# Optimization experiments

Measured on AMD Instinct MI355X. Metric: run time of the kernel, lower is better.

The kernel has to match this reference:

```python
import jax, jax.numpy as jnp
import numpy as np

B, T, N = 1024, 5, 6        # batch, seq_len (fixed by conv3d1 kernel), max_node_num
D, E, M, L = 192, 12, 12, 512  # node feat, edge feat, message size, link hidden
P = 2                        # propagate_layers
O = 6                        # big_attr_classes / conv3d out channels


def setup_inputs() -> dict:
    key = jax.random.key(0)
    ks = jax.random.split(key, 16)
    w = lambda k, shp: jax.random.normal(k, shp, jnp.float32) * 0.02
    return {
        "node_resnet": jax.random.normal(ks[0], (B, T, D, N), jnp.float32),
        "pos": jax.random.normal(ks[1], (B, T, N, 6), jnp.float32),
        "attmat": jax.random.randint(ks[2], (B, T, N, N), 0, 2).astype(jnp.int32),
        "link_w1": w(ks[3], (L, E)), "link_b1": jnp.zeros((L,), jnp.float32),
        "link_w2": w(ks[4], (1, L)), "link_b2": jnp.zeros((1,), jnp.float32),
        "msg_Wh": w(ks[5], (M, D)), "msg_We": w(ks[6], (M, E)), "msg_b": jnp.zeros((M,), jnp.float32),
        "gru_Wih": w(ks[7], (3 * D, M)), "gru_Whh": w(ks[8], (3 * D, D)),
        "gru_bih": jnp.zeros((3 * D,), jnp.float32), "gru_bhh": jnp.zeros((3 * D,), jnp.float32),
        "conv1_w": w(ks[9], (O, D, T, N, 1)), "conv1_b": jnp.zeros((O,), jnp.float32),
        "conv2_w": w(ks[10], (O, O)), "conv2_b": jnp.zeros((O,), jnp.float32),
    }


def reference(node_resnet, pos, attmat, link_w1, link_b1, link_w2, link_b2,
              msg_Wh, msg_We, msg_b, gru_Wih, gru_Whh, gru_bih, gru_bhh,
              conv1_w, conv1_b, conv2_w, conv2_b):
    # edge features: e[b,t,:,i,j] = cat(pos_i, pos_j) where ATTMAT==1 and i!=j
    eye = jnp.eye(N, dtype=bool)
    mask = (attmat == 1) & (~eye)[None, None]                      # [B,T,N,N]
    pi = jnp.broadcast_to(pos[:, :, :, None, :], (B, T, N, N, 6))
    pj = jnp.broadcast_to(pos[:, :, None, :, :], (B, T, N, N, 6))
    e = jnp.concatenate([pi, pj], -1) * mask[..., None]            # [B,T,N,N,E]
    e = jnp.moveaxis(e, -1, 2)                                     # [B,T,E,N,N]

    def link(es):  # GraphConv link function: 1x1 conv stack -> scalar edge logit
        hmid = jax.nn.relu(jnp.einsum('btcij,oc->btoij', es, link_w1)
                           + link_b1[None, None, :, None, None])
        return jnp.einsum('btoij,po->btpij', hmid, link_w2)[:, :, 0] + link_b2[0]  # [B,T,N,N]

    h = node_resnet                                                # [B,T,D,N]
    edge_state = e
    for _ in range(P):
        adj = jax.nn.sigmoid(link(edge_state))                     # [B,T,N,N] gate (i=target, j=source)
        # message: relu(Wh h_j + We e_ij + b), gated by sigmoid adjacency
        mh = jnp.einsum('btcj,oc->btoj', h, msg_Wh)                # [B,T,M,N]
        me = jnp.einsum('btcij,oc->btoij', e, msg_We)              # [B,T,M,N,N]
        m = jax.nn.relu(mh[:, :, :, None, :] + me + msg_b[None, None, :, None, None])
        m = adj[:, :, None, :, :] * m                              # gated messages
        edge_state = m                                             # next-round edge hidden state
        msum = m.sum(-1)                                           # aggregate over source j: [B,T,M,N]
        # GRU update per node (PyTorch gate order r, z, n)
        x = jnp.moveaxis(msum, 2, -1)                              # [B,T,N,M]
        hh = jnp.moveaxis(h, 2, -1)                                # [B,T,N,D]
        gi = x @ gru_Wih.T + gru_bih
        gh = hh @ gru_Whh.T + gru_bhh
        ir, iz, inn = jnp.split(gi, 3, -1)
        hr, hz, hn = jnp.split(gh, 3, -1)
        r = jax.nn.sigmoid(ir + hr)
        z = jax.nn.sigmoid(iz + hz)
        n = jnp.tanh(inn + r * hn)
        hh = (1.0 - z) * n + z * hh
        h = jnp.moveaxis(hh, -1, 2)                                # [B,T,D,N]

    # conv3d1 kernel (5,6,1) spans full (T,N) -> single contraction per batch
    out = jax.nn.relu(jnp.einsum('btdn,odtn->bo', h, conv1_w[..., 0]) + conv1_b)
    out = out @ conv2_w.T + conv2_b                                # conv3d2 is 1x1x1
    return out.reshape(B, O, 1, 1, 1)
```

## Files before the change

### kernel.cpp

```cpp
#include <hip/hip_runtime.h>
#include <math.h>

#define NB 1024
#define TT 5
#define NN 6
#define DD 192
#define EE 12
#define MM 12
#define LL 512
#define OO 6
#define GOUT 768
#define KPAD 224
#define NKT (KPAD/32)
#define NJT (GOUT/16)

#define ROWS 30
#define HP 196
#define LNKPU 20
#define GRUPU 116

typedef __attribute__((ext_vector_type(8))) _Float16 f16x8;
typedef __attribute__((ext_vector_type(2))) _Float16 h2;
typedef __attribute__((ext_vector_type(4))) float f32x4;

__device__ __forceinline__ float dot4(float4 a, float4 b) {
  return a.x*b.x + a.y*b.y + a.z*b.z + a.w*b.w;
}
__device__ __forceinline__ unsigned short f2h(float f) {
  _Float16 h = (_Float16)f;
  unsigned short s; __builtin_memcpy(&s, &h, 2); return s;
}
__device__ __forceinline__ unsigned int pkrtz(float a, float b) {
  auto v = __builtin_amdgcn_cvt_pkrtz(a, b);
  return __builtin_bit_cast(unsigned int, v);
}
__device__ __forceinline__ float fsig(float x) {
  float e = __expf(-x);
  return __builtin_amdgcn_rcpf(1.f + e);
}
__device__ __forceinline__ float ftanh(float x) {
  float e = __expf(-2.f * x);
  return 2.f * __builtin_amdgcn_rcpf(1.f + e) - 1.f;
}

__global__ void k_pack(const float* __restrict__ Wih, const float* __restrict__ Whh,
                       const float* __restrict__ bih, const float* __restrict__ bhh,
                       unsigned short* __restrict__ Bh, float* __restrict__ bias768)
{
  int idx = blockIdx.x * 256 + threadIdx.x;
  if (idx < GOUT) {
    int c = idx; float b;
    if (c < 384)      b = bih[c] + bhh[c];
    else if (c < 576) b = bih[c];
    else              b = bhh[c - 192];
    bias768[c] = b;
  }
  if (idx >= NJT*NKT*512) return;
  int e = idx & 7, l = (idx >> 3) & 63;
  int rem = idx >> 9, kt = rem % NKT, j = rem / NKT;
  int k = kt*32 + ((l >> 4) << 3) + e;
  int c = j*16 + (l & 15);
  float v = 0.f;
  if (k < 204) {
    if (c < 384)      v = (k < 12) ? Wih[c*MM + k] : Whh[(size_t)c*DD + (k-12)];
    else if (c < 576) v = (k < 12) ? Wih[c*MM + k] : 0.f;
    else              v = (k < 12) ? 0.f : Whh[(size_t)(c-192)*DD + (k-12)];
  }
  Bh[idx] = f2h(v);
}

__global__ void k_pack_link(const float* __restrict__ w1, const float* __restrict__ b1,
                            unsigned short* __restrict__ BLh)
{
  int idx = blockIdx.x * 256 + threadIdx.x;
  if (idx >= 32*512) return;
  int e = idx & 7, l = (idx >> 3) & 63, nt = idx >> 9;
  int k = ((l >> 4) << 3) + e;
  int c = nt*16 + (l & 15);
  float v = 0.f;
  if (k < 12)       v = w1[c*EE + k];
  else if (k == 12) v = b1[c];
  BLh[idx] = f2h(v);
}

__global__ __launch_bounds__(256, 2)
void k_fused(const float* __restrict__ nr, const float* __restrict__ pos,
             const int* __restrict__ attmat,
             const unsigned short* __restrict__ BLh,
             const float* __restrict__ lw2, const float* __restrict__ lb2,
             const float* __restrict__ msg_Wh, const float* __restrict__ msg_We,
             const float* __restrict__ msg_b,
             const unsigned short* __restrict__ Bh, const float* __restrict__ bias768,
             const float* __restrict__ conv1_w, const float* __restrict__ conv1_b,
             const float* __restrict__ conv2_w, const float* __restrict__ conv2_b,
             float* __restrict__ out)
{
  __shared__ __align__(16) float sh_h[ROWS][HP];
  __shared__ __align__(16) unsigned int sh_e[180][6];
  __shared__ __align__(16) unsigned int sh_m[180][6];
  __shared__ __align__(16) float sh_mh[ROWS][MM];
  __shared__ float sh_adj[192];
  __shared__ float sh_w2[LL];
  __shared__ __align__(16) unsigned int sh_we[MM][6];
  __shared__ __align__(16) unsigned int shA[192*LNKPU];
  __shared__ float red[4][OO];

  const int tid = threadIdx.x;
  const int b = blockIdx.x;
  const int lane = tid & 63, wid = tid >> 6;
  const int col = lane & 15, quad = lane >> 4;

  for (int i = tid; i < TT*DD*NN; i += 256) {
    int t = i / (DD*NN), rem = i % (DD*NN);
    int d = rem / NN, n = rem % NN;
    sh_h[t*NN + n][d] = nr[(size_t)b*TT*DD*NN + i];
  }
  for (int idx = tid; idx < 180*6; idx += 256) {
    int e = idx / 6, p = idx % 6;
    int t = e / 36, ij = e % 36;
    int i_ = ij / NN, j_ = ij % NN;
    bool msk = (attmat[(b*TT + t)*36 + ij] == 1) && (i_ != j_);
    int srcn = (p < 3) ? i_ : j_;
    int c0   = (p < 3) ? 2*p : 2*p - 6;
    const float* pb = pos + (((size_t)(b*TT + t))*NN + srcn)*6;
    float a0 = msk ? pb[c0] : 0.f, a1 = msk ? pb[c0+1] : 0.f;
    sh_e[e][p] = pkrtz(a0, a1);
  }
  for (int idx = tid; idx < MM*6; idx += 256) {
    int o = idx / 6, p = idx % 6;
    sh_we[o][p] = pkrtz(msg_We[o*EE + 2*p], msg_We[o*EE + 2*p + 1]);
  }
  for (int i = tid; i < LL; i += 256) sh_w2[i] = lw2[i];
  __syncthreads();

  for (int L = 0; L < 2; ++L) {
    for (int idx = tid; idx < 192*16; idx += 256) {
      int r = idx >> 4, p = idx & 15;
      unsigned int v = 0;
      if (r < 180) {
        if (p < 6)       v = (L == 0) ? sh_e[r][p] : sh_m[r][p];
        else if (p == 6) v = 0x00003C00u;
      }
      shA[r*LNKPU + p] = v;
    }
    __syncthreads();

    {
      f16x8 am[3];
      #pragma unroll
      for (int mtl = 0; mtl < 3; ++mtl)
        am[mtl] = *(const f16x8*)((const char*)shA
                    + ((wid*3 + mtl)*16 + col)*(LNKPU*4) + quad*16);
      float s[3][4];
      #pragma unroll
      for (int mtl = 0; mtl < 3; ++mtl)
        #pragma unroll
        for (int q = 0; q < 4; ++q) s[mtl][q] = 0.f;
      for (int nt = 0; nt < 32; ++nt) {
        f16x8 bh = *(const f16x8*)(BLh + nt*512 + lane*8);
        float w2v = sh_w2[nt*16 + col];
        #pragma unroll
        for (int mtl = 0; mtl < 3; ++mtl) {
          f32x4 acc = (f32x4)0.f;
          acc = __builtin_amdgcn_mfma_f32_16x16x32_f16(am[mtl], bh, acc, 0, 0, 0);
          #pragma unroll
          for (int q = 0; q < 4; ++q)
            s[mtl][q] += w2v * fmaxf(acc[q], 0.f);
        }
      }
      #pragma unroll
      for (int mtl = 0; mtl < 3; ++mtl)
        #pragma unroll
        for (int q = 0; q < 4; ++q) {
          float v = s[mtl][q];
          v += __shfl_xor(v, 1); v += __shfl_xor(v, 2);
          v += __shfl_xor(v, 4); v += __shfl_xor(v, 8);
          s[mtl][q] = v;
        }
      if (col == 0) {
        float b2 = lb2[0];
        #pragma unroll
        for (int mtl = 0; mtl < 3; ++mtl)
          #pragma unroll
          for (int q = 0; q < 4; ++q)
            sh_adj[wid*48 + mtl*16 + quad*4 + q] = fsig(s[mtl][q] + b2);
      }
    }
    __syncthreads();

    for (int idx = tid; idx < ROWS*MM; idx += 256) {
      int r = idx / MM, o = idx % MM;
      const float4* wrow = (const float4*)(msg_Wh + (size_t)o*DD);
      const float4* hrow = (const float4*)&sh_h[r][0];
      float acc = msg_b[o];
      #pragma unroll 8
      for (int d4 = 0; d4 < DD/4; ++d4) acc += dot4(wrow[d4], hrow[d4]);
      sh_mh[r][o] = acc;
    }
    __syncthreads();

    for (int idx = tid; idx < 180*6; idx += 256) {
      int e = idx / 6, op = idx % 6;
      int t = e / 36, j_ = e % 6;
      h2 a2 = {(_Float16)0.f, (_Float16)0.f};
      h2 b2 = {(_Float16)0.f, (_Float16)0.f};
      #pragma unroll
      for (int p = 0; p < 6; ++p) {
        h2 ev = __builtin_bit_cast(h2, sh_e[e][p]);
        a2 += __builtin_bit_cast(h2, sh_we[2*op][p]) * ev;
        b2 += __builtin_bit_cast(h2, sh_we[2*op+1][p]) * ev;
      }
      float me0 = (float)a2[0] + (float)a2[1];
      float me1 = (float)b2[0] + (float)b2[1];
      float mh0 = sh_mh[t*NN + j_][2*op];
      float mh1 = sh_mh[t*NN + j_][2*op+1];
      float adj = sh_adj[e];
      sh_m[e][op] = pkrtz(adj * fmaxf(mh0 + me0, 0.f),
                          adj * fmaxf(mh1 + me1, 0.f));
    }
    __syncthreads();

    for (int idx = tid; idx < 32*(KPAD/2); idx += 256) {
      int r = idx / (KPAD/2), kp = idx % (KPAD/2);
      unsigned int v = 0;
      if (r < ROWS) {
        if (kp < 6) {
          int t = r / NN, i_ = r % NN;
          const unsigned int* mrow = &sh_m[t*36 + i_*NN][kp];
          float a0 = 0.f, a1 = 0.f;
          #pragma unroll
          for (int j = 0; j < 6; ++j) {
            h2 mv = __builtin_bit_cast(h2, mrow[j*6]);
            a0 += (float)mv[0]; a1 += (float)mv[1];
          }
          v = pkrtz(a0, a1);
        } else if (kp < 102) {
          float2 hv = *(const float2*)&sh_h[r][2*kp - 12];
          v = pkrtz(hv.x, hv.y);
        }
      }
      shA[r*GRUPU + kp] = v;
    }
    __syncthreads();

    {
      const char* ahb = (const char*)shA + col*(GRUPU*4) + quad*16;
      #pragma unroll 1
      for (int i = 0; i < 3; ++i) {
        const int jR = wid*3 + i;
        const int jZ = 12 + wid*3 + i;
        const int jI = 24 + wid*3 + i;
        const int jH = 36 + wid*3 + i;
        f32x4 aR0 = (f32x4)0.f, aR1 = (f32x4)0.f;
        f32x4 aZ0 = (f32x4)0.f, aZ1 = (f32x4)0.f;
        f32x4 aI0 = (f32x4)0.f, aI1 = (f32x4)0.f;
        f32x4 aH0 = (f32x4)0.f, aH1 = (f32x4)0.f;
        #pragma unroll
        for (int kt = 0; kt < NKT; ++kt) {
          f16x8 ah0 = *(const f16x8*)(ahb + kt*64);
          f16x8 ah1 = *(const f16x8*)(ahb + 16*(GRUPU*4) + kt*64);
          f16x8 bR = *(const f16x8*)(Bh + (((size_t)(jR*NKT + kt)) << 9) + lane*8);
          f16x8 bZ = *(const f16x8*)(Bh + (((size_t)(jZ*NKT + kt)) << 9) + lane*8);
          f16x8 bH = *(const f16x8*)(Bh + (((size_t)(jH*NKT + kt)) << 9) + lane*8);
          aR0 = __builtin_amdgcn_mfma_f32_16x16x32_f16(ah0, bR, aR0, 0, 0, 0);
          aR1 = __builtin_amdgcn_mfma_f32_16x16x32_f16(ah1, bR, aR1, 0, 0, 0);
          aZ0 = __builtin_amdgcn_mfma_f32_16x16x32_f16(ah0, bZ, aZ0, 0, 0, 0);
          aZ1 = __builtin_amdgcn_mfma_f32_16x16x32_f16(ah1, bZ, aZ1, 0, 0, 0);
          aH0 = __builtin_amdgcn_mfma_f32_16x16x32_f16(ah0, bH, aH0, 0, 0, 0);
          aH1 = __builtin_amdgcn_mfma_f32_16x16x32_f16(ah1, bH, aH1, 0, 0, 0);
          if (kt == 0) {
            f16x8 bI = *(const f16x8*)(Bh + (((size_t)(jI*NKT)) << 9) + lane*8);
            aI0 = __builtin_amdgcn_mfma_f32_16x16x32_f16(ah0, bI, aI0, 0, 0, 0);
            aI1 = __builtin_amdgcn_mfma_f32_16x16x32_f16(ah1, bI, aI1, 0, 0, 0);
          }
        }
        const int d = (wid*3 + i)*16 + col;
        const float bR_ = bias768[d],       bZ_ = bias768[192 + d];
        const float bI_ = bias768[384 + d], bH_ = bias768[576 + d];
        #pragma unroll
        for (int q = 0; q < 4; ++q) {
          const int g0 = quad*4 + q;
          float r_ = fsig(aR0[q] + bR_);
          float z_ = fsig(aZ0[q] + bZ_);
          float n_ = ftanh(aI0[q] + bI_ + r_*(aH0[q] + bH_));
          float hold = sh_h[g0][d];
          sh_h[g0][d] = (1.f - z_)*n_ + z_*hold;
        }
        #pragma unroll
        for (int q = 0; q < 4; ++q) {
          const int g1 = 16 + quad*4 + q;
          if (g1 < ROWS) {
            float r_ = fsig(aR1[q] + bR_);
            float z_ = fsig(aZ1[q] + bZ_);
            float n_ = ftanh(aI1[q] + bI_ + r_*(aH1[q] + bH_));
            float hold = sh_h[g1][d];
            sh_h[g1][d] = (1.f - z_)*n_ + z_*hold;
          }
        }
      }
    }
    __syncthreads();
  }

  {
    float acco[OO];
    #pragma unroll
    for (int o = 0; o < OO; ++o) acco[o] = 0.f;
    for (int u = tid; u < DD*TT*NN; u += 256) {
      int r = u % ROWS, c = u / ROWS;
      float hv = sh_h[r][c];
      #pragma unroll
      for (int o = 0; o < OO; ++o)
        acco[o] += conv1_w[o*(DD*TT*NN) + u] * hv;
    }
    #pragma unroll
    for (int o = 0; o < OO; ++o) {
      float v = acco[o];
      v += __shfl_xor(v, 1);  v += __shfl_xor(v, 2);  v += __shfl_xor(v, 4);
      v += __shfl_xor(v, 8);  v += __shfl_xor(v, 16); v += __shfl_xor(v, 32);
      acco[o] = v;
    }
    if (lane == 0) {
      #pragma unroll
      for (int o = 0; o < OO; ++o) red[wid][o] = acco[o];
    }
    __syncthreads();
    if (tid == 0) {
      float y[OO];
      #pragma unroll
      for (int o = 0; o < OO; ++o) {
        float s = conv1_b[o] + red[0][o] + red[1][o] + red[2][o] + red[3][o];
        y[o] = fmaxf(s, 0.f);
      }
      #pragma unroll
      for (int q = 0; q < OO; ++q) {
        float s = conv2_b[q];
        #pragma unroll
        for (int o = 0; o < OO; ++o) s += conv2_w[q*OO + o] * y[o];
        out[b*OO + q] = s;
      }
    }
  }
}

extern "C" void kernel_launch(void* const* d_in, const int* in_sizes, int n_in,
                              void* d_out, int out_size, void* d_ws, size_t ws_size,
                              hipStream_t stream) {
  const float* node_resnet = (const float*)d_in[0];
  const float* pos      = (const float*)d_in[1];
  const int*   attmat   = (const int*)  d_in[2];
  const float* link_w1  = (const float*)d_in[3];
  const float* link_b1  = (const float*)d_in[4];
  const float* link_w2  = (const float*)d_in[5];
  const float* link_b2  = (const float*)d_in[6];
  const float* msg_Wh   = (const float*)d_in[7];
  const float* msg_We   = (const float*)d_in[8];
  const float* msg_b    = (const float*)d_in[9];
  const float* gru_Wih  = (const float*)d_in[10];
  const float* gru_Whh  = (const float*)d_in[11];
  const float* gru_bih  = (const float*)d_in[12];
  const float* gru_bhh  = (const float*)d_in[13];
  const float* conv1_w  = (const float*)d_in[14];
  const float* conv1_b  = (const float*)d_in[15];
  const float* conv2_w  = (const float*)d_in[16];
  const float* conv2_b  = (const float*)d_in[17];
  float* out = (float*)d_out;

  float* bias = (float*)d_ws;
  unsigned short* Bh  = (unsigned short*)(bias + GOUT);
  unsigned short* BLh = Bh + (size_t)NJT*NKT*512;

  k_pack<<<(NJT*NKT*512 + 255)/256, 256, 0, stream>>>(gru_Wih, gru_Whh,
      gru_bih, gru_bhh, Bh, bias);
  k_pack_link<<<(32*512 + 255)/256, 256, 0, stream>>>(link_w1, link_b1, BLh);
  k_fused<<<NB, 256, 0, stream>>>(node_resnet, pos, attmat,
      BLh, link_w2, link_b2,
      msg_Wh, msg_We, msg_b,
      Bh, bias,
      conv1_w, conv1_b, conv2_w, conv2_b, out);
}
```

Baseline: 156.1 us.

## Drop shared staging buffers, read MFMA fragments directly, raise occupancy

The shared staging buffers (shA, sh_w2) for the link and GRU MFMA inputs are removed. Link A-fragments are now read straight from padded sh_e/sh_m rows. GRU A-fragments are built on the fly from fp32 sh_h and a new small message-sum buffer, with the K ordering rearranged so h comes first and x last. The GRU weight pack skips zero K-tiles for the n-gate halves, and results are held in registers and written back after a barrier. Launch bounds rise from 2 to 4 blocks per CU. Together these cut LDS footprint and staging passes, at the cost of more register pressure and repeated fp32-to-fp16 conversion per tile.

```diff
diff --git a/kernel.cpp b/kernel.cpp
--- a/kernel.cpp
+++ b/kernel.cpp
@@ -13,11 +13,8 @@
 #define KPAD 224
 #define NKT (KPAD/32)
 #define NJT (GOUT/16)
-
 #define ROWS 30
 #define HP 196
-#define LNKPU 20
-#define GRUPU 116
 
 typedef __attribute__((ext_vector_type(8))) _Float16 f16x8;
 typedef __attribute__((ext_vector_type(2))) _Float16 h2;
@@ -41,6 +38,13 @@
 __device__ __forceinline__ float ftanh(float x) {
   float e = __expf(-2.f * x);
   return 2.f * __builtin_amdgcn_rcpf(1.f + e) - 1.f;
+}
+__device__ __forceinline__ f16x8 frag8(const float* p) {
+  float4 a = *(const float4*)p;
+  float4 b = *(const float4*)(p + 4);
+  uint4 u = make_uint4(pkrtz(a.x, a.y), pkrtz(a.z, a.w),
+                       pkrtz(b.x, b.y), pkrtz(b.z, b.w));
+  return __builtin_bit_cast(f16x8, u);
 }
 
 __global__ void k_pack(const float* __restrict__ Wih, const float* __restrict__ Whh,
@@ -61,10 +65,13 @@
   int k = kt*32 + ((l >> 4) << 3) + e;
   int c = j*16 + (l & 15);
   float v = 0.f;
-  if (k < 204) {
-    if (c < 384)      v = (k < 12) ? Wih[c*MM + k] : Whh[(size_t)c*DD + (k-12)];
-    else if (c < 576) v = (k < 12) ? Wih[c*MM + k] : 0.f;
-    else              v = (k < 12) ? 0.f : Whh[(size_t)(c-192)*DD + (k-12)];
+  if (k < 192) {
+    if (c < 384)      v = Whh[(size_t)c*DD + k];
+    else if (c < 576) v = 0.f;
+    else              v = Whh[(size_t)(c-192)*DD + k];
+  } else if (k < 204) {
+    if (c < 576)      v = Wih[c*MM + (k - 192)];
+    else              v = 0.f;
   }
   Bh[idx] = f2h(v);
 }
@@ -83,7 +90,63 @@
   BLh[idx] = f2h(v);
 }
 
-__global__ __launch_bounds__(256, 2)
+struct NH8 { float v[8]; };
+
+#define GRU_TILE(I, NHO)                                                        \
+  {                                                                             \
+    const int jR = wid*3 + (I);                                                 \
+    const int jZ = 12 + wid*3 + (I);                                            \
+    const int jI = 24 + wid*3 + (I);                                            \
+    const int jH = 36 + wid*3 + (I);                                            \
+    f32x4 aR0=(f32x4)0.f, aR1=(f32x4)0.f, aZ0=(f32x4)0.f, aZ1=(f32x4)0.f;       \
+    f32x4 aI0=(f32x4)0.f, aI1=(f32x4)0.f, aH0=(f32x4)0.f, aH1=(f32x4)0.f;       \
+    _Pragma("unroll")                                                           \
+    for (int kt = 0; kt < NKT; ++kt) {                                          \
+      f16x8 ah0, ah1;                                                           \
+      if (kt < 6) {                                                             \
+        ah0 = frag8(h0row + kt*32 + quad*8);                                    \
+        ah1 = frag8(h1row + kt*32 + quad*8);                                    \
+      } else {                                                                  \
+        f16x8 zf = __builtin_bit_cast(f16x8, make_uint4(0u,0u,0u,0u));          \
+        ah0 = (quad == 3) ? zf : frag8(x0row + quad*8);                         \
+        ah1 = (quad == 3) ? zf : frag8(x1row + quad*8);                         \
+      }                                                                         \
+      f16x8 bR = *(const f16x8*)(Bh + (((size_t)(jR*NKT + kt)) << 9) + lane*8); \
+      f16x8 bZ = *(const f16x8*)(Bh + (((size_t)(jZ*NKT + kt)) << 9) + lane*8); \
+      aR0 = __builtin_amdgcn_mfma_f32_16x16x32_f16(ah0, bR, aR0, 0, 0, 0);      \
+      aR1 = __builtin_amdgcn_mfma_f32_16x16x32_f16(ah1, bR, aR1, 0, 0, 0);      \
+      aZ0 = __builtin_amdgcn_mfma_f32_16x16x32_f16(ah0, bZ, aZ0, 0, 0, 0);      \
+      aZ1 = __builtin_amdgcn_mfma_f32_16x16x32_f16(ah1, bZ, aZ1, 0, 0, 0);      \
+      if (kt < 6) {                                                             \
+        f16x8 bH = *(const f16x8*)(Bh + (((size_t)(jH*NKT + kt)) << 9) + lane*8); \
+        aH0 = __builtin_amdgcn_mfma_f32_16x16x32_f16(ah0, bH, aH0, 0, 0, 0);    \
+        aH1 = __builtin_amdgcn_mfma_f32_16x16x32_f16(ah1, bH, aH1, 0, 0, 0);    \
+      } else {                                                                  \
+        f16x8 bI = *(const f16x8*)(Bh + (((size_t)(jI*NKT + kt)) << 9) + lane*8); \
+        aI0 = __builtin_amdgcn_mfma_f32_16x16x32_f16(ah0, bI, aI0, 0, 0, 0);    \
+        aI1 = __builtin_amdgcn_mfma_f32_16x16x32_f16(ah1, bI, aI1, 0, 0, 0);    \
+      }                                                                         \
+    }                                                                           \
+    const int d = (wid*3 + (I))*16 + col;                                       \
+    const float bR_ = bias768[d],       bZ_ = bias768[192 + d];                 \
+    const float bI_ = bias768[384 + d], bH_ = bias768[576 + d];                 \
+    _Pragma("unroll")                                                           \
+    for (int q = 0; q < 4; ++q) {                                               \
+      int g0 = quad*4 + q;                                                      \
+      float r_ = fsig(aR0[q] + bR_);                                            \
+      float z_ = fsig(aZ0[q] + bZ_);                                            \
+      float n_ = ftanh(aI0[q] + bI_ + r_*(aH0[q] + bH_));                       \
+      NHO.v[q] = (1.f - z_)*n_ + z_*sh_h[g0][d];                                \
+      int g1 = 16 + quad*4 + q;                                                 \
+      float r1_ = fsig(aR1[q] + bR_);                                           \
+      float z1_ = fsig(aZ1[q] + bZ_);                                           \
+      float n1_ = ftanh(aI1[q] + bI_ + r1_*(aH1[q] + bH_));                     \
+      float hold1 = (g1 < ROWS) ? sh_h[g1][d] : 0.f;                            \
+      NHO.v[4+q] = (1.f - z1_)*n1_ + z1_*hold1;                                 \
+    }                                                                           \
+  }
+
+__global__ __launch_bounds__(256, 4)
 void k_fused(const float* __restrict__ nr, const float* __restrict__ pos,
              const int* __restrict__ attmat,
              const unsigned short* __restrict__ BLh,
@@ -96,13 +159,12 @@
              float* __restrict__ out)
 {
   __shared__ __align__(16) float sh_h[ROWS][HP];
-  __shared__ __align__(16) unsigned int sh_e[180][6];
-  __shared__ __align__(16) unsigned int sh_m[180][6];
+  __shared__ __align__(16) unsigned int sh_e[180][8];
+  __shared__ __align__(16) unsigned int sh_m[180][8];
   __shared__ __align__(16) float sh_mh[ROWS][MM];
+  __shared__ __align__(16) float sh_msum[ROWS][24];
   __shared__ float sh_adj[192];
-  __shared__ float sh_w2[LL];
   __shared__ __align__(16) unsigned int sh_we[MM][6];
-  __shared__ __align__(16) unsigned int shA[192*LNKPU];
   __shared__ float red[4][OO];
 
   const int tid = threadIdx.x;
@@ -115,42 +177,41 @@
     int d = rem / NN, n = rem % NN;
     sh_h[t*NN + n][d] = nr[(size_t)b*TT*DD*NN + i];
   }
-  for (int idx = tid; idx < 180*6; idx += 256) {
-    int e = idx / 6, p = idx % 6;
-    int t = e / 36, ij = e % 36;
-    int i_ = ij / NN, j_ = ij % NN;
-    bool msk = (attmat[(b*TT + t)*36 + ij] == 1) && (i_ != j_);
-    int srcn = (p < 3) ? i_ : j_;
-    int c0   = (p < 3) ? 2*p : 2*p - 6;
-    const float* pb = pos + (((size_t)(b*TT + t))*NN + srcn)*6;
-    float a0 = msk ? pb[c0] : 0.f, a1 = msk ? pb[c0+1] : 0.f;
-    sh_e[e][p] = pkrtz(a0, a1);
+  for (int idx = tid; idx < 180*8; idx += 256) {
+    int e = idx >> 3, p = idx & 7;
+    unsigned int v = 0;
+    if (p < 6) {
+      int t = e / 36, ij = e % 36;
+      int i_ = ij / NN, j_ = ij % NN;
+      bool msk = (attmat[(b*TT + t)*36 + ij] == 1) && (i_ != j_);
+      int srcn = (p < 3) ? i_ : j_;
+      int c0   = (p < 3) ? 2*p : 2*p - 6;
+      const float* pb = pos + (((size_t)(b*TT + t))*NN + srcn)*6;
+      float a0 = msk ? pb[c0] : 0.f, a1 = msk ? pb[c0+1] : 0.f;
+      v = pkrtz(a0, a1);
+    } else if (p == 6) {
+      v = 0x00003C00u;
+    }
+    sh_e[e][p] = v;
+    if (p >= 6) sh_m[e][p] = v;
   }
   for (int idx = tid; idx < MM*6; idx += 256) {
     int o = idx / 6, p = idx % 6;
     sh_we[o][p] = pkrtz(msg_We[o*EE + 2*p], msg_We[o*EE + 2*p + 1]);
   }
-  for (int i = tid; i < LL; i += 256) sh_w2[i] = lw2[i];
   __syncthreads();
 
   for (int L = 0; L < 2; ++L) {
-    for (int idx = tid; idx < 192*16; idx += 256) {
-      int r = idx >> 4, p = idx & 15;
-      unsigned int v = 0;
-      if (r < 180) {
-        if (p < 6)       v = (L == 0) ? sh_e[r][p] : sh_m[r][p];
-        else if (p == 6) v = 0x00003C00u;
-      }
-      shA[r*LNKPU + p] = v;
-    }
-    __syncthreads();
-
     {
       f16x8 am[3];
       #pragma unroll
-      for (int mtl = 0; mtl < 3; ++mtl)
-        am[mtl] = *(const f16x8*)((const char*)shA
-                    + ((wid*3 + mtl)*16 + col)*(LNKPU*4) + quad*16);
+      for (int mtl = 0; mtl < 3; ++mtl) {
+        int r = (wid*3 + mtl)*16 + col; r = r > 179 ? 179 : r;
+        const unsigned int* src = (L == 0) ? &sh_e[r][0] : &sh_m[r][0];
+        uint4 w = make_uint4(0u,0u,0u,0u);
+        if (quad < 2) w = *(const uint4*)(src + quad*4);
+        am[mtl] = __builtin_bit_cast(f16x8, w);
+      }
       float s[3][4];
       #pragma unroll
       for (int mtl = 0; mtl < 3; ++mtl)
@@ -158,7 +219,7 @@
         for (int q = 0; q < 4; ++q) s[mtl][q] = 0.f;
       for (int nt = 0; nt < 32; ++nt) {
         f16x8 bh = *(const f16x8*)(BLh + nt*512 + lane*8);
-        float w2v = sh_w2[nt*16 + col];
+        float w2v = lw2[nt*16 + col];
         #pragma unroll
         for (int mtl = 0; mtl < 3; ++mtl) {
           f32x4 acc = (f32x4)0.f;
@@ -220,81 +281,47 @@
     }
     __syncthreads();
 
-    for (int idx = tid; idx < 32*(KPAD/2); idx += 256) {
-      int r = idx / (KPAD/2), kp = idx % (KPAD/2);
-      unsigned int v = 0;
-      if (r < ROWS) {
-        if (kp < 6) {
-          int t = r / NN, i_ = r % NN;
-          const unsigned int* mrow = &sh_m[t*36 + i_*NN][kp];
-          float a0 = 0.f, a1 = 0.f;
-          #pragma unroll
-          for (int j = 0; j < 6; ++j) {
-            h2 mv = __builtin_bit_cast(h2, mrow[j*6]);
-            a0 += (float)mv[0]; a1 += (float)mv[1];
-          }
-          v = pkrtz(a0, a1);
-        } else if (kp < 102) {
-          float2 hv = *(const float2*)&sh_h[r][2*kp - 12];
-          v = pkrtz(hv.x, hv.y);
+    for (int idx = tid; idx < ROWS*24; idx += 256) {
+      int r = idx / 24, o = idx % 24;
+      float s = 0.f;
+      if (o < 12) {
+        int t = r / NN, i_ = r % NN;
+        #pragma unroll
+        for (int j = 0; j < 6; ++j) {
+          h2 mv = __builtin_bit_cast(h2, sh_m[t*36 + i_*NN + j][o >> 1]);
+          s += (float)mv[o & 1];
         }
       }
-      shA[r*GRUPU + kp] = v;
+      sh_msum[r][o] = s;
     }
     __syncthreads();
 
     {
-      const char* ahb = (const char*)shA + col*(GRUPU*4) + quad*16;
-      #pragma unroll 1
-      for (int i = 0; i < 3; ++i) {
-        const int jR = wid*3 + i;
-        const int jZ = 12 + wid*3 + i;
-        const int jI = 24 + wid*3 + i;
-        const int jH = 36 + wid*3 + i;
-        f32x4 aR0 = (f32x4)0.f, aR1 = (f32x4)0.f;
-        f32x4 aZ0 = (f32x4)0.f, aZ1 = (f32x4)0.f;
-        f32x4 aI0 = (f32x4)0.f, aI1 = (f32x4)0.f;
-        f32x4 aH0 = (f32x4)0.f, aH1 = (f32x4)0.f;
-        #pragma unroll
-        for (int kt = 0; kt < NKT; ++kt) {
-          f16x8 ah0 = *(const f16x8*)(ahb + kt*64);
-          f16x8 ah1 = *(const f16x8*)(ahb + 16*(GRUPU*4) + kt*64);
-          f16x8 bR = *(const f16x8*)(Bh + (((size_t)(jR*NKT + kt)) << 9) + lane*8);
-          f16x8 bZ = *(const f16x8*)(Bh + (((size_t)(jZ*NKT + kt)) << 9) + lane*8);
-          f16x8 bH = *(const f16x8*)(Bh + (((size_t)(jH*NKT + kt)) << 9) + lane*8);
-          aR0 = __builtin_amdgcn_mfma_f32_16x16x32_f16(ah0, bR, aR0, 0, 0, 0);
-          aR1 = __builtin_amdgcn_mfma_f32_16x16x32_f16(ah1, bR, aR1, 0, 0, 0);
-          aZ0 = __builtin_amdgcn_mfma_f32_16x16x32_f16(ah0, bZ, aZ0, 0, 0, 0);
-          aZ1 = __builtin_amdgcn_mfma_f32_16x16x32_f16(ah1, bZ, aZ1, 0, 0, 0);
-          aH0 = __builtin_amdgcn_mfma_f32_16x16x32_f16(ah0, bH, aH0, 0, 0, 0);
-          aH1 = __builtin_amdgcn_mfma_f32_16x16x32_f16(ah1, bH, aH1, 0, 0, 0);
-          if (kt == 0) {
-            f16x8 bI = *(const f16x8*)(Bh + (((size_t)(jI*NKT)) << 9) + lane*8);
-            aI0 = __builtin_amdgcn_mfma_f32_16x16x32_f16(ah0, bI, aI0, 0, 0, 0);
-            aI1 = __builtin_amdgcn_mfma_f32_16x16x32_f16(ah1, bI, aI1, 0, 0, 0);
-          }
-        }
-        const int d = (wid*3 + i)*16 + col;
-        const float bR_ = bias768[d],       bZ_ = bias768[192 + d];
-        const float bI_ = bias768[384 + d], bH_ = bias768[576 + d];
+      const float* h0row = &sh_h[col][0];
+      int r1c = col + 16; if (r1c > 29) r1c = 29;
+      const float* h1row = &sh_h[r1c][0];
+      const float* x0row = &sh_msum[col][0];
+      const float* x1row = &sh_msum[r1c][0];
+      NH8 nh0, nh1, nh2;
+      GRU_TILE(0, nh0)
+      GRU_TILE(1, nh1)
+      GRU_TILE(2, nh2)
+      __syncthreads();
+      {
+        const int d0 = (wid*3 + 0)*16 + col;
+        const int d1 = (wid*3 + 1)*16 + col;
+        const int d2 = (wid*3 + 2)*16 + col;
         #pragma unroll
         for (int q = 0; q < 4; ++q) {
-          const int g0 = quad*4 + q;
-          float r_ = fsig(aR0[q] + bR_);
-          float z_ = fsig(aZ0[q] + bZ_);
-          float n_ = ftanh(aI0[q] + bI_ + r_*(aH0[q] + bH_));
-          float hold = sh_h[g0][d];
-          sh_h[g0][d] = (1.f - z_)*n_ + z_*hold;
-        }
-        #pragma unroll
-        for (int q = 0; q < 4; ++q) {
-          const int g1 = 16 + quad*4 + q;
+          int g0 = quad*4 + q;
+          sh_h[g0][d0] = nh0.v[q];
+          sh_h[g0][d1] = nh1.v[q];
+          sh_h[g0][d2] = nh2.v[q];
+          int g1 = 16 + quad*4 + q;
           if (g1 < ROWS) {
-            float r_ = fsig(aR1[q] + bR_);
-            float z_ = fsig(aZ1[q] + bZ_);
-            float n_ = ftanh(aI1[q] + bI_ + r_*(aH1[q] + bH_));
-            float hold = sh_h[g1][d];
-            sh_h[g1][d] = (1.f - z_)*n_ + z_*hold;
+            sh_h[g1][d0] = nh0.v[4+q];
+            sh_h[g1][d1] = nh1.v[4+q];
+            sh_h[g1][d2] = nh2.v[4+q];
           }
         }
       }
```

Result: slower. 300.1 us (+92.2%).

## Shrink LDS footprint: drop link staging buffer, halve GRU A tile, fp16 scratch

Applied to the files above, without the earlier changes.

The link-function A operand is now built straight from the edge/message arrays in registers, which removes the 192-row staging buffer and its extra barrier. The link bias moves from a padded K column into an add inside the epilogue. The GRU step is split into two 16-row halves so its A tile needs only 16 rows of shared memory, and the message and adjacency scratch are stored as fp16. The aim is to cut per-block LDS so more blocks can reside per CU. The cost is a second GRU pass that re-reads the weights and adds barriers, plus link w2 and b1 now read from global memory inside the inner loop.

```diff
diff --git a/kernel.cpp b/kernel.cpp
--- a/kernel.cpp
+++ b/kernel.cpp
@@ -13,10 +13,8 @@
 #define KPAD 224
 #define NKT (KPAD/32)
 #define NJT (GOUT/16)
-
 #define ROWS 30
 #define HP 196
-#define LNKPU 20
 #define GRUPU 116
 
 typedef __attribute__((ext_vector_type(8))) _Float16 f16x8;
@@ -29,6 +27,9 @@
 __device__ __forceinline__ unsigned short f2h(float f) {
   _Float16 h = (_Float16)f;
   unsigned short s; __builtin_memcpy(&s, &h, 2); return s;
+}
+__device__ __forceinline__ float h2f(unsigned short s) {
+  _Float16 h; __builtin_memcpy(&h, &s, 2); return (float)h;
 }
 __device__ __forceinline__ unsigned int pkrtz(float a, float b) {
   auto v = __builtin_amdgcn_cvt_pkrtz(a, b);
@@ -69,7 +70,7 @@
   Bh[idx] = f2h(v);
 }
 
-__global__ void k_pack_link(const float* __restrict__ w1, const float* __restrict__ b1,
+__global__ void k_pack_link(const float* __restrict__ w1,
                             unsigned short* __restrict__ BLh)
 {
   int idx = blockIdx.x * 256 + threadIdx.x;
@@ -77,17 +78,15 @@
   int e = idx & 7, l = (idx >> 3) & 63, nt = idx >> 9;
   int k = ((l >> 4) << 3) + e;
   int c = nt*16 + (l & 15);
-  float v = 0.f;
-  if (k < 12)       v = w1[c*EE + k];
-  else if (k == 12) v = b1[c];
-  BLh[idx] = f2h(v);
+  BLh[idx] = f2h((k < 12) ? w1[c*EE + k] : 0.f);
 }
 
 __global__ __launch_bounds__(256, 2)
 void k_fused(const float* __restrict__ nr, const float* __restrict__ pos,
              const int* __restrict__ attmat,
              const unsigned short* __restrict__ BLh,
-             const float* __restrict__ lw2, const float* __restrict__ lb2,
+             const float* __restrict__ lb1, const float* __restrict__ lw2,
+             const float* __restrict__ lb2,
              const float* __restrict__ msg_Wh, const float* __restrict__ msg_We,
              const float* __restrict__ msg_b,
              const unsigned short* __restrict__ Bh, const float* __restrict__ bias768,
@@ -98,12 +97,10 @@
   __shared__ __align__(16) float sh_h[ROWS][HP];
   __shared__ __align__(16) unsigned int sh_e[180][6];
   __shared__ __align__(16) unsigned int sh_m[180][6];
-  __shared__ __align__(16) float sh_mh[ROWS][MM];
-  __shared__ float sh_adj[192];
-  __shared__ float sh_w2[LL];
+  __shared__ __align__(16) unsigned int shA[16*GRUPU];
+  __shared__ __align__(16) unsigned short sh_mh[ROWS][MM];
   __shared__ __align__(16) unsigned int sh_we[MM][6];
-  __shared__ __align__(16) unsigned int shA[192*LNKPU];
-  __shared__ float red[4][OO];
+  __shared__ unsigned short sh_adj[180];
 
   const int tid = threadIdx.x;
   const int b = blockIdx.x;
@@ -130,27 +127,26 @@
     int o = idx / 6, p = idx % 6;
     sh_we[o][p] = pkrtz(msg_We[o*EE + 2*p], msg_We[o*EE + 2*p + 1]);
   }
-  for (int i = tid; i < LL; i += 256) sh_w2[i] = lw2[i];
   __syncthreads();
 
   for (int L = 0; L < 2; ++L) {
-    for (int idx = tid; idx < 192*16; idx += 256) {
-      int r = idx >> 4, p = idx & 15;
-      unsigned int v = 0;
-      if (r < 180) {
-        if (p < 6)       v = (L == 0) ? sh_e[r][p] : sh_m[r][p];
-        else if (p == 6) v = 0x00003C00u;
-      }
-      shA[r*LNKPU + p] = v;
-    }
-    __syncthreads();
-
     {
       f16x8 am[3];
       #pragma unroll
-      for (int mtl = 0; mtl < 3; ++mtl)
-        am[mtl] = *(const f16x8*)((const char*)shA
-                    + ((wid*3 + mtl)*16 + col)*(LNKPU*4) + quad*16);
+      for (int mtl = 0; mtl < 3; ++mtl) {
+        int r = (wid*3 + mtl)*16 + col; r = r > 179 ? 179 : r;
+        const unsigned int* src = (L == 0) ? &sh_e[r][0] : &sh_m[r][0];
+        uint4 w = make_uint4(0u, 0u, 0u, 0u);
+        if (quad == 0) {
+          uint2 lo = *(const uint2*)(src);
+          uint2 hi = *(const uint2*)(src + 2);
+          w = make_uint4(lo.x, lo.y, hi.x, hi.y);
+        } else if (quad == 1) {
+          uint2 lo = *(const uint2*)(src + 4);
+          w = make_uint4(lo.x, lo.y, 0u, 0u);
+        }
+        am[mtl] = __builtin_bit_cast(f16x8, w);
+      }
       float s[3][4];
       #pragma unroll
       for (int mtl = 0; mtl < 3; ++mtl)
@@ -158,14 +154,15 @@
         for (int q = 0; q < 4; ++q) s[mtl][q] = 0.f;
       for (int nt = 0; nt < 32; ++nt) {
         f16x8 bh = *(const f16x8*)(BLh + nt*512 + lane*8);
-        float w2v = sh_w2[nt*16 + col];
+        float b1v = lb1[nt*16 + col];
+        float w2v = lw2[nt*16 + col];
         #pragma unroll
         for (int mtl = 0; mtl < 3; ++mtl) {
           f32x4 acc = (f32x4)0.f;
           acc = __builtin_amdgcn_mfma_f32_16x16x32_f16(am[mtl], bh, acc, 0, 0, 0);
           #pragma unroll
           for (int q = 0; q < 4; ++q)
-            s[mtl][q] += w2v * fmaxf(acc[q], 0.f);
+            s[mtl][q] += w2v * fmaxf(acc[q] + b1v, 0.f);
         }
       }
       #pragma unroll
@@ -182,8 +179,10 @@
         #pragma unroll
         for (int mtl = 0; mtl < 3; ++mtl)
           #pragma unroll
-          for (int q = 0; q < 4; ++q)
-            sh_adj[wid*48 + mtl*16 + quad*4 + q] = fsig(s[mtl][q] + b2);
+          for (int q = 0; q < 4; ++q) {
+            int e = wid*48 + mtl*16 + quad*4 + q;
+            if (e < 180) sh_adj[e] = f2h(fsig(s[mtl][q] + b2));
+          }
       }
     }
     __syncthreads();
@@ -195,7 +194,7 @@
       float acc = msg_b[o];
       #pragma unroll 8
       for (int d4 = 0; d4 < DD/4; ++d4) acc += dot4(wrow[d4], hrow[d4]);
-      sh_mh[r][o] = acc;
+      sh_mh[r][o] = f2h(acc);
     }
     __syncthreads();
 
@@ -212,97 +211,86 @@
       }
       float me0 = (float)a2[0] + (float)a2[1];
       float me1 = (float)b2[0] + (float)b2[1];
-      float mh0 = sh_mh[t*NN + j_][2*op];
-      float mh1 = sh_mh[t*NN + j_][2*op+1];
-      float adj = sh_adj[e];
+      float mh0 = h2f(sh_mh[t*NN + j_][2*op]);
+      float mh1 = h2f(sh_mh[t*NN + j_][2*op + 1]);
+      float adj = h2f(sh_adj[e]);
       sh_m[e][op] = pkrtz(adj * fmaxf(mh0 + me0, 0.f),
                           adj * fmaxf(mh1 + me1, 0.f));
     }
     __syncthreads();
 
-    for (int idx = tid; idx < 32*(KPAD/2); idx += 256) {
-      int r = idx / (KPAD/2), kp = idx % (KPAD/2);
-      unsigned int v = 0;
-      if (r < ROWS) {
-        if (kp < 6) {
-          int t = r / NN, i_ = r % NN;
-          const unsigned int* mrow = &sh_m[t*36 + i_*NN][kp];
-          float a0 = 0.f, a1 = 0.f;
+    #pragma unroll 1
+    for (int H = 0; H < 2; ++H) {
+      for (int idx = tid; idx < 16*(KPAD/2); idx += 256) {
+        int r = idx / (KPAD/2), kp = idx % (KPAD/2);
+        int grow = H*16 + r;
+        unsigned int v = 0;
+        if (grow < ROWS) {
+          if (kp < 6) {
+            int t = grow / NN, i_ = grow % NN;
+            const unsigned int* mrow = &sh_m[t*36 + i_*NN][kp];
+            float a0 = 0.f, a1 = 0.f;
+            #pragma unroll
+            for (int j = 0; j < 6; ++j) {
+              h2 mv = __builtin_bit_cast(h2, mrow[j*6]);
+              a0 += (float)mv[0]; a1 += (float)mv[1];
+            }
+            v = pkrtz(a0, a1);
+          } else if (kp < 102) {
+            float2 hv = *(const float2*)&sh_h[grow][2*kp - 12];
+            v = pkrtz(hv.x, hv.y);
+          }
+        }
+        shA[r*GRUPU + kp] = v;
+      }
+      __syncthreads();
+
+      {
+        const char* ahb = (const char*)shA + col*(GRUPU*4) + quad*16;
+        #pragma unroll 1
+        for (int i = 0; i < 3; ++i) {
+          const int jR = wid*3 + i;
+          const int jZ = 12 + wid*3 + i;
+          const int jI = 24 + wid*3 + i;
+          const int jH = 36 + wid*3 + i;
+          f32x4 aR = (f32x4)0.f, aZ = (f32x4)0.f;
+          f32x4 aI = (f32x4)0.f, aH = (f32x4)0.f;
           #pragma unroll
-          for (int j = 0; j < 6; ++j) {
-            h2 mv = __builtin_bit_cast(h2, mrow[j*6]);
-            a0 += (float)mv[0]; a1 += (float)mv[1];
+          for (int kt = 0; kt < NKT; ++kt) {
+            f16x8 ah = *(const f16x8*)(ahb + kt*64);
+            f16x8 bR = *(const f16x8*)(Bh + (((size_t)(jR*NKT + kt)) << 9) + lane*8);
+            f16x8 bZ = *(const f16x8*)(Bh + (((size_t)(jZ*NKT + kt)) << 9) + lane*8);
+            f16x8 bH = *(const f16x8*)(Bh + (((size_t)(jH*NKT + kt)) << 9) + lane*8);
+            aR = __builtin_amdgcn_mfma_f32_16x16x32_f16(ah, bR, aR, 0, 0, 0);
+            aZ = __builtin_amdgcn_mfma_f32_16x16x32_f16(ah, bZ, aZ, 0, 0, 0);
+            aH = __builtin_amdgcn_mfma_f32_16x16x32_f16(ah, bH, aH, 0, 0, 0);
+            if (kt == 0) {
+              f16x8 bI = *(const f16x8*)(Bh + (((size_t)(jI*NKT)) << 9) + lane*8);
+              aI = __builtin_amdgcn_mfma_f32_16x16x32_f16(ah, bI, aI, 0, 0, 0);
+            }
           }
-          v = pkrtz(a0, a1);
-        } else if (kp < 102) {
-          float2 hv = *(const float2*)&sh_h[r][2*kp - 12];
-          v = pkrtz(hv.x, hv.y);
-        }
-      }
-      shA[r*GRUPU + kp] = v;
-    }
-    __syncthreads();
-
-    {
-      const char* ahb = (const char*)shA + col*(GRUPU*4) + quad*16;
-      #pragma unroll 1
-      for (int i = 0; i < 3; ++i) {
-        const int jR = wid*3 + i;
-        const int jZ = 12 + wid*3 + i;
-        const int jI = 24 + wid*3 + i;
-        const int jH = 36 + wid*3 + i;
-        f32x4 aR0 = (f32x4)0.f, aR1 = (f32x4)0.f;
-        f32x4 aZ0 = (f32x4)0.f, aZ1 = (f32x4)0.f;
-        f32x4 aI0 = (f32x4)0.f, aI1 = (f32x4)0.f;
-        f32x4 aH0 = (f32x4)0.f, aH1 = (f32x4)0.f;
-        #pragma unroll
-        for (int kt = 0; kt < NKT; ++kt) {
-          f16x8 ah0 = *(const f16x8*)(ahb + kt*64);
-          f16x8 ah1 = *(const f16x8*)(ahb + 16*(GRUPU*4) + kt*64);
-          f16x8 bR = *(const f16x8*)(Bh + (((size_t)(jR*NKT + kt)) << 9) + lane*8);
-          f16x8 bZ = *(const f16x8*)(Bh + (((size_t)(jZ*NKT + kt)) << 9) + lane*8);
-          f16x8 bH = *(const f16x8*)(Bh + (((size_t)(jH*NKT + kt)) << 9) + lane*8);
-          aR0 = __builtin_amdgcn_mfma_f32_16x16x32_f16(ah0, bR, aR0, 0, 0, 0);
-          aR1 = __builtin_amdgcn_mfma_f32_16x16x32_f16(ah1, bR, aR1, 0, 0, 0);
-          aZ0 = __builtin_amdgcn_mfma_f32_16x16x32_f16(ah0, bZ, aZ0, 0, 0, 0);
-          aZ1 = __builtin_amdgcn_mfma_f32_16x16x32_f16(ah1, bZ, aZ1, 0, 0, 0);
-          aH0 = __builtin_amdgcn_mfma_f32_16x16x32_f16(ah0, bH, aH0, 0, 0, 0);
-          aH1 = __builtin_amdgcn_mfma_f32_16x16x32_f16(ah1, bH, aH1, 0, 0, 0);
-          if (kt == 0) {
-            f16x8 bI = *(const f16x8*)(Bh + (((size_t)(jI*NKT)) << 9) + lane*8);
-            aI0 = __builtin_amdgcn_mfma_f32_16x16x32_f16(ah0, bI, aI0, 0, 0, 0);
-            aI1 = __builtin_amdgcn_mfma_f32_16x16x32_f16(ah1, bI, aI1, 0, 0, 0);
+          const int d = (wid*3 + i)*16 + col;
+          const float bR_ = bias768[d],       bZ_ = bias768[192 + d];
+          const float bI_ = bias768[384 + d], bH_ = bias768[576 + d];
+          #pragma unroll
+          for (int q = 0; q < 4; ++q) {
+            const int grow = H*16 + quad*4 + q;
+            if (grow < ROWS) {
+              float r_ = fsig(aR[q] + bR_);
+              float z_ = fsig(aZ[q] + bZ_);
+              float n_ = ftanh(aI[q] + bI_ + r_*(aH[q] + bH_));
+              float hold = sh_h[grow][d];
+              sh_h[grow][d] = (1.f - z_)*n_ + z_*hold;
+            }
           }
         }
-        const int d = (wid*3 + i)*16 + col;
-        const float bR_ = bias768[d],       bZ_ = bias768[192 + d];
-        const float bI_ = bias768[384 + d], bH_ = bias768[576 + d];
-        #pragma unroll
-        for (int q = 0; q < 4; ++q) {
-          const int g0 = quad*4 + q;
-          float r_ = fsig(aR0[q] + bR_);
-          float z_ = fsig(aZ0[q] + bZ_);
-          float n_ = ftanh(aI0[q] + bI_ + r_*(aH0[q] + bH_));
-          float hold = sh_h[g0][d];
-          sh_h[g0][d] = (1.f - z_)*n_ + z_*hold;
-        }
-        #pragma unroll
-        for (int q = 0; q < 4; ++q) {
-          const int g1 = 16 + quad*4 + q;
-          if (g1 < ROWS) {
-            float r_ = fsig(aR1[q] + bR_);
-            float z_ = fsig(aZ1[q] + bZ_);
-            float n_ = ftanh(aI1[q] + bI_ + r_*(aH1[q] + bH_));
-            float hold = sh_h[g1][d];
-            sh_h[g1][d] = (1.f - z_)*n_ + z_*hold;
-          }
-        }
-      }
-    }
-    __syncthreads();
+      }
+      __syncthreads();
+    }
   }
 
   {
+    float* red = (float*)&sh_mh[0][0];
     float acco[OO];
     #pragma unroll
     for (int o = 0; o < OO; ++o) acco[o] = 0.f;
@@ -320,16 +308,17 @@
       v += __shfl_xor(v, 8);  v += __shfl_xor(v, 16); v += __shfl_xor(v, 32);
       acco[o] = v;
     }
+    __syncthreads();
     if (lane == 0) {
       #pragma unroll
-      for (int o = 0; o < OO; ++o) red[wid][o] = acco[o];
+      for (int o = 0; o < OO; ++o) red[wid*OO + o] = acco[o];
     }
     __syncthreads();
     if (tid == 0) {
       float y[OO];
       #pragma unroll
       for (int o = 0; o < OO; ++o) {
-        float s = conv1_b[o] + red[0][o] + red[1][o] + red[2][o] + red[3][o];
+        float s = conv1_b[o] + red[0*OO+o] + red[1*OO+o] + red[2*OO+o] + red[3*OO+o];
         y[o] = fmaxf(s, 0.f);
       }
       #pragma unroll
@@ -372,9 +361,9 @@
 
   k_pack<<<(NJT*NKT*512 + 255)/256, 256, 0, stream>>>(gru_Wih, gru_Whh,
       gru_bih, gru_bhh, Bh, bias);
-  k_pack_link<<<(32*512 + 255)/256, 256, 0, stream>>>(link_w1, link_b1, BLh);
+  k_pack_link<<<(32*512 + 255)/256, 256, 0, stream>>>(link_w1, BLh);
   k_fused<<<NB, 256, 0, stream>>>(node_resnet, pos, attmat,
-      BLh, link_w2, link_b2,
+      BLh, link_b1, link_w2, link_b2,
       msg_Wh, msg_We, msg_b,
       Bh, bias,
       conv1_w, conv1_b, conv2_w, conv2_b, out);
```

Measured after the change: 142.1 us, median of 2. 9.0% less time.
